# Optimization experiments

Hardware: AMD Instinct MI355X
Metric: run time of the kernel (lower is better)

Reference implementation:

```python
import jax, jax.numpy as jnp
import numpy as np

NUM_LAYERS = 3
DROPOUT = 0.0  # set to 0 for deterministic reference (torch F.dropout uses its own RNG)


def _spmm(rows, cols, vals, X, n_rows):
    # sparse [n_rows, n_cols] @ X[n_cols, D] via gather + segment_sum
    return jax.ops.segment_sum(vals[:, None] * X[cols], rows, num_segments=n_rows)


def setup_inputs() -> dict:
    key = jax.random.key(0)
    k1, k2, k3, k4, k5 = jax.random.split(key, 5)
    P, U, NNZ, D = 100000, 50000, 2000000, 128
    pois_embs = jax.random.normal(k1, (P, D), dtype=jnp.float32)
    up_rows = jax.random.randint(k2, (NNZ,), 0, U, dtype=jnp.int32)
    up_cols = jax.random.randint(k3, (NNZ,), 0, P, dtype=jnp.int32)
    up_vals = jax.random.uniform(k4, (NNZ,), dtype=jnp.float32)
    pu_vals = jax.random.uniform(k5, (NNZ,), dtype=jnp.float32)
    return {
        "pois_embs": pois_embs,
        "pad_all_train_sessions": jnp.zeros((1,), dtype=jnp.int64),
        "up_rows": up_rows,
        "up_cols": up_cols,
        "up_vals": up_vals,
        "pu_vals": pu_vals,
        "n_users": U,
        "n_pois": P,
    }


def reference(pois_embs, pad_all_train_sessions, up_rows, up_cols, up_vals, pu_vals, n_users, n_pois):
    # HG_up: [U, P] with entries (up_rows, up_cols, up_vals)
    # HG_pu: [P, U] = transpose structure with values pu_vals
    x = pois_embs
    acc = pois_embs  # running sum over layer outputs (incl. layer 0)
    for _ in range(NUM_LAYERS):
        msg = _spmm(up_rows, up_cols, up_vals, x, n_users)          # [U, D]
        prop = _spmm(up_cols, up_rows, pu_vals, msg, n_pois)        # [P, D]
        x = prop + x                                                 # residual
        # dropout with p=DROPOUT=0.0 -> identity
        acc = acc + x
    return acc / jnp.asarray(NUM_LAYERS + 1, dtype=pois_embs.dtype)
```

## Files before the change

### kernel.cpp

```cpp
#include <hip/hip_runtime.h>

#define DD 128
#define NUM_LAYERS 3
#define SCAN_B 1024
#define BKT_SHIFT 7
#define BKT_ROWS 128
#define LDS_BKT 1280
#define EPB 4096
#define SHARDS 4
#define CAP_SUB 1792

typedef unsigned int uint;

__device__ __forceinline__ uint f2bf(float f) {
    uint u = __float_as_uint(f);
    return (u + 0x7fffu + ((u >> 16) & 1u)) >> 16;
}
__device__ __forceinline__ uint pk2(float a, float b) {
    return f2bf(a) | (f2bf(b) << 16);
}
__device__ __forceinline__ void fma8(float acc[8], uint4 q, float v) {
    acc[0] += v * __uint_as_float(q.x << 16);
    acc[1] += v * __uint_as_float(q.x & 0xffff0000u);
    acc[2] += v * __uint_as_float(q.y << 16);
    acc[3] += v * __uint_as_float(q.y & 0xffff0000u);
    acc[4] += v * __uint_as_float(q.z << 16);
    acc[5] += v * __uint_as_float(q.z & 0xffff0000u);
    acc[6] += v * __uint_as_float(q.w << 16);
    acc[7] += v * __uint_as_float(q.w & 0xffff0000u);
}


__global__ void pass1_kernel(const int* __restrict__ up_rows,
                             const int* __restrict__ up_cols,
                             const float* __restrict__ up_vals,
                             const float* __restrict__ pu_vals,
                             int* __restrict__ bkcur,
                             int2* __restrict__ stage,
                             int nnz, int U, int nbkt) {
    __shared__ int lcnt[LDS_BKT];
    const int tid = threadIdx.x;
    const int e0 = blockIdx.x * EPB;
    const int shard = blockIdx.x & (SHARDS - 1);
    for (int i = tid; i < nbkt; i += 256) lcnt[i] = 0;
    __syncthreads();
    #pragma unroll
    for (int i = 0; i < EPB / 256; ++i) {
        const int e = e0 + i * 256 + tid;
        if (e < nnz) {
            atomicAdd(&lcnt[up_rows[e] >> BKT_SHIFT], 1);
            atomicAdd(&lcnt[(U + up_cols[e]) >> BKT_SHIFT], 1);
        }
    }
    __syncthreads();
    for (int i = tid; i < nbkt; i += 256) {
        const int c = lcnt[i];
        lcnt[i] = c ? atomicAdd(&bkcur[i * SHARDS + shard], c) : 0;
    }
    __syncthreads();
    #pragma unroll
    for (int i = 0; i < EPB / 256; ++i) {
        const int e = e0 + i * 256 + tid;
        if (e < nnz) {
            const int u = up_rows[e];
            const int p = up_cols[e];
            const int pc = U + p;
            int b = u >> BKT_SHIFT;
            int pos = atomicAdd(&lcnt[b], 1);
            if (pos < CAP_SUB)
                stage[((size_t)b * SHARDS + shard) * CAP_SUB + pos] =
                    make_int2(((u & (BKT_ROWS - 1)) << 25) | p, __float_as_int(up_vals[e]));
            b = pc >> BKT_SHIFT;
            pos = atomicAdd(&lcnt[b], 1);
            if (pos < CAP_SUB)
                stage[((size_t)b * SHARDS + shard) * CAP_SUB + pos] =
                    make_int2(((pc & (BKT_ROWS - 1)) << 25) | u, __float_as_int(pu_vals[e]));
        }
    }
}

__global__ void hist2_kernel(const int* __restrict__ bkcur,
                             const int2* __restrict__ stage,
                             int* __restrict__ cnt, int N) {
    __shared__ int lc[BKT_ROWS];
    const int b = blockIdx.x;
    if (threadIdx.x < BKT_ROWS) lc[threadIdx.x] = 0;
    __syncthreads();
    for (int s = 0; s < SHARDS; ++s) {
        const int n = min(bkcur[b * SHARDS + s], CAP_SUB);
        const int2* bs = stage + ((size_t)b * SHARDS + s) * CAP_SUB;
        for (int i = threadIdx.x; i < n; i += blockDim.x)
            atomicAdd(&lc[((uint)bs[i].x) >> 25], 1);
    }
    __syncthreads();
    const int r = b * BKT_ROWS + threadIdx.x;
    if (threadIdx.x < BKT_ROWS && r < N) cnt[r] = lc[threadIdx.x];
}

__global__ void scan_blocks_kernel(const int* __restrict__ in, int* __restrict__ out,
                                   int* __restrict__ bsums, int n) {
    __shared__ int tmp[SCAN_B];
    const int tid = threadIdx.x;
    const int gid = blockIdx.x * SCAN_B + tid;
    const int v = (gid < n) ? in[gid] : 0;
    tmp[tid] = v;
    __syncthreads();
    for (int ofs = 1; ofs < SCAN_B; ofs <<= 1) {
        int t = (tid >= ofs) ? tmp[tid - ofs] : 0;
        __syncthreads();
        tmp[tid] += t;
        __syncthreads();
    }
    if (gid < n) out[gid] = tmp[tid] - v;
    if (tid == SCAN_B - 1) bsums[blockIdx.x] = tmp[tid];
}

__global__ void scan_sums_kernel(int* __restrict__ bsums, int nb) {
    __shared__ int tmp[SCAN_B];
    const int tid = threadIdx.x;
    const int v = (tid < nb) ? bsums[tid] : 0;
    tmp[tid] = v;
    __syncthreads();
    for (int ofs = 1; ofs < SCAN_B; ofs <<= 1) {
        int t = (tid >= ofs) ? tmp[tid - ofs] : 0;
        __syncthreads();
        tmp[tid] += t;
        __syncthreads();
    }
    if (tid < nb) bsums[tid] = tmp[tid] - v;
}

__global__ void scan_add_kernel(int* __restrict__ off, const int* __restrict__ bsums,
                                const int* __restrict__ cnt, int n) {
    const int gid = blockIdx.x * SCAN_B + threadIdx.x;
    if (gid >= n) return;
    const int v = off[gid] + bsums[blockIdx.x];
    off[gid] = v;
    if (gid == n - 1) off[n] = v + cnt[gid];
}

__global__ void pass2_kernel(const int* __restrict__ bkcur,
                             const int2* __restrict__ stage,
                             const int* __restrict__ off,
                             int2* __restrict__ adj, int N) {
    __shared__ int lcur[BKT_ROWS];
    const int b = blockIdx.x;
    const int r = b * BKT_ROWS + threadIdx.x;
    if (threadIdx.x < BKT_ROWS) lcur[threadIdx.x] = (r < N) ? off[r] : 0;
    __syncthreads();
    for (int s = 0; s < SHARDS; ++s) {
        const int n = min(bkcur[b * SHARDS + s], CAP_SUB);
        const int2* bs = stage + ((size_t)b * SHARDS + s) * CAP_SUB;
        for (int i = threadIdx.x; i < n; i += blockDim.x) {
            const int2 ev = bs[i];
            const uint rl = ((uint)ev.x) >> 25;
            const int col = ev.x & 0x1ffffff;
            const int pos = atomicAdd(&lcur[rl], 1);
            adj[pos] = make_int2(col, ev.y);
        }
    }
}

__global__ void cvt_kernel(const float4* __restrict__ src, uint2* __restrict__ dst, int n4) {
    const int i = blockIdx.x * blockDim.x + threadIdx.x;
    if (i >= n4) return;
    const float4 f = src[i];
    dst[i] = make_uint2(pk2(f.x, f.y), pk2(f.z, f.w));
}


__global__ void spmm_u_kernel(const int* __restrict__ off,
                              const int2* __restrict__ adj,
                              const uint4* __restrict__ xbf,
                              uint4* __restrict__ msgbf, int U) {
    const int g = threadIdx.x >> 4;
    const int lane = threadIdx.x & 15;
    const int row = blockIdx.x * 16 + g;
    if (row >= U) return;
    int k = off[row];
    const int end = off[row + 1];
    float acc[8] = {0, 0, 0, 0, 0, 0, 0, 0};
    for (; k + 1 < end; k += 2) {
        const int2 e0 = adj[k];
        const int2 e1 = adj[k + 1];
        const uint4 q0 = xbf[(size_t)e0.x * 16 + lane];
        const uint4 q1 = xbf[(size_t)e1.x * 16 + lane];
        fma8(acc, q0, __int_as_float(e0.y));
        fma8(acc, q1, __int_as_float(e1.y));
    }
    if (k < end) {
        const int2 e0 = adj[k];
        const uint4 q0 = xbf[(size_t)e0.x * 16 + lane];
        fma8(acc, q0, __int_as_float(e0.y));
    }
    uint4 o;
    o.x = pk2(acc[0], acc[1]);
    o.y = pk2(acc[2], acc[3]);
    o.z = pk2(acc[4], acc[5]);
    o.w = pk2(acc[6], acc[7]);
    msgbf[(size_t)row * 16 + lane] = o;
}

__global__ void spmm_p_fused_kernel(const int* __restrict__ off,
                                    const int2* __restrict__ adj,
                                    const uint4* __restrict__ msgbf,
                                    uint4* __restrict__ xbf,
                                    const float4* __restrict__ embs,
                                    float4* __restrict__ out,
                                    float w, int first, int last, int U, int P) {
    const int g = threadIdx.x >> 4;
    const int lane = threadIdx.x & 15;
    const int row = blockIdx.x * 16 + g;
    if (row >= P) return;
    int k = off[U + row];
    const int end = off[U + row + 1];
    float acc[8] = {0, 0, 0, 0, 0, 0, 0, 0};
    for (; k + 1 < end; k += 2) {
        const int2 e0 = adj[k];
        const int2 e1 = adj[k + 1];
        const uint4 q0 = msgbf[(size_t)e0.x * 16 + lane];
        const uint4 q1 = msgbf[(size_t)e1.x * 16 + lane];
        fma8(acc, q0, __int_as_float(e0.y));
        fma8(acc, q1, __int_as_float(e1.y));
    }
    if (k < end) {
        const int2 e0 = adj[k];
        const uint4 q0 = msgbf[(size_t)e0.x * 16 + lane];
        fma8(acc, q0, __int_as_float(e0.y));
    }
    const size_t xi = (size_t)row * 16 + lane;
    if (!last) {
        const uint4 xq = xbf[xi];
        uint4 xn;
        xn.x = pk2(__uint_as_float(xq.x << 16) + acc[0],
                   __uint_as_float(xq.x & 0xffff0000u) + acc[1]);
        xn.y = pk2(__uint_as_float(xq.y << 16) + acc[2],
                   __uint_as_float(xq.y & 0xffff0000u) + acc[3]);
        xn.z = pk2(__uint_as_float(xq.z << 16) + acc[4],
                   __uint_as_float(xq.z & 0xffff0000u) + acc[5]);
        xn.w = pk2(__uint_as_float(xq.w << 16) + acc[6],
                   __uint_as_float(xq.w & 0xffff0000u) + acc[7]);
        xbf[xi] = xn;
    }
    const size_t oi = (size_t)row * 32 + lane * 2;
    const float4* base = first ? embs : (const float4*)out;
    float4 a = base[oi];
    float4 b = base[oi + 1];
    a.x += w * acc[0]; a.y += w * acc[1]; a.z += w * acc[2]; a.w += w * acc[3];
    b.x += w * acc[4]; b.y += w * acc[5]; b.z += w * acc[6]; b.w += w * acc[7];
    out[oi] = a;
    out[oi + 1] = b;
}


extern "C" void kernel_launch(void* const* d_in, const int* in_sizes, int n_in,
                              void* d_out, int out_size, void* d_ws, size_t ws_size,
                              hipStream_t stream) {
    const float* embs    = (const float*)d_in[0];
    const int*   up_rows = (const int*)d_in[2];
    const int*   up_cols = (const int*)d_in[3];
    const float* up_vals = (const float*)d_in[4];
    const float* pu_vals = (const float*)d_in[5];

    const int NNZ = in_sizes[2];
    const int P   = in_sizes[0] / DD;
    const int U   = 50000;
    const int N   = U + P;
    const int NBKT = (N + BKT_ROWS - 1) / BKT_ROWS;

    float* out = (float*)d_out;

    char* ws = (char*)d_ws;
    size_t o = 0;
    auto alloc = [&](size_t bytes) { size_t r = o; o = (o + bytes + 255) & ~255ULL; return r; };
    int*  bkcur = (int*) (ws + alloc((size_t)NBKT * SHARDS * 4));
    int*  cnt   = (int*) (ws + alloc((size_t)N * 4));
    int*  off   = (int*) (ws + alloc((size_t)(N + 1) * 4));
    int*  bsums = (int*) (ws + alloc((size_t)SCAN_B * 4));
    int2* adj   = (int2*)(ws + alloc((size_t)2 * NNZ * 8));
    const size_t stage_off = alloc((size_t)NBKT * SHARDS * CAP_SUB * 8);
    int2*  stage = (int2*)(ws + stage_off);
    uint4* xbf   = (uint4*)(ws + stage_off);
    uint4* msgbf = (uint4*)(ws + stage_off + (size_t)P * DD * 2);

    const int NB = (N + SCAN_B - 1) / SCAN_B;

    hipMemsetAsync(bkcur, 0, (size_t)NBKT * SHARDS * 4, stream);
    const int p1blocks = (NNZ + EPB - 1) / EPB;
    pass1_kernel<<<p1blocks, 256, 0, stream>>>(up_rows, up_cols, up_vals, pu_vals,
                                               bkcur, stage, NNZ, U, NBKT);
    hist2_kernel<<<NBKT, 256, 0, stream>>>(bkcur, stage, cnt, N);
    scan_blocks_kernel<<<NB, SCAN_B, 0, stream>>>(cnt, off, bsums, N);
    scan_sums_kernel<<<1, SCAN_B, 0, stream>>>(bsums, NB);
    scan_add_kernel<<<NB, SCAN_B, 0, stream>>>(off, bsums, cnt, N);
    pass2_kernel<<<NBKT, 256, 0, stream>>>(bkcur, stage, off, adj, N);

    const int n4 = P * DD / 4;
    cvt_kernel<<<(n4 + 255) / 256, 256, 0, stream>>>((const float4*)embs, (uint2*)xbf, n4);

    const int ublocks = (U + 15) / 16;
    const int pblocks = (P + 15) / 16;

    for (int layer = 0; layer < NUM_LAYERS; ++layer) {
        const float w = (float)(NUM_LAYERS - layer) / (NUM_LAYERS + 1);
        spmm_u_kernel<<<ublocks, 256, 0, stream>>>(off, adj, xbf, msgbf, U);
        spmm_p_fused_kernel<<<pblocks, 256, 0, stream>>>(
            off, adj, msgbf, xbf, (const float4*)embs, (float4*)out,
            w, layer == 0, layer == NUM_LAYERS - 1, U, P);
    }
}
```

Before: 605.6 us.

## Scan per-bucket totals and fuse row histogram into pass2; unroll SpMM gathers by four

Removes the separate per-row histogram pass over the staged edges. The global scan now runs over bucket totals (about 1.2K entries instead of 150K rows), and pass2 computes its per-row counts and local prefix in LDS, writing the CSR offsets itself. The SpMM row loops are also unrolled from 2 to 4 gathers to put more loads in flight, at the cost of more registers per thread. Stage is still read twice, but both reads now happen inside one kernel.

```diff
diff --git a/kernel.cpp b/kernel.cpp
--- a/kernel.cpp
+++ b/kernel.cpp
@@ -79,22 +79,14 @@
     }
 }
 
-__global__ void hist2_kernel(const int* __restrict__ bkcur,
-                             const int2* __restrict__ stage,
-                             int* __restrict__ cnt, int N) {
-    __shared__ int lc[BKT_ROWS];
-    const int b = blockIdx.x;
-    if (threadIdx.x < BKT_ROWS) lc[threadIdx.x] = 0;
-    __syncthreads();
-    for (int s = 0; s < SHARDS; ++s) {
-        const int n = min(bkcur[b * SHARDS + s], CAP_SUB);
-        const int2* bs = stage + ((size_t)b * SHARDS + s) * CAP_SUB;
-        for (int i = threadIdx.x; i < n; i += blockDim.x)
-            atomicAdd(&lc[((uint)bs[i].x) >> 25], 1);
-    }
-    __syncthreads();
-    const int r = b * BKT_ROWS + threadIdx.x;
-    if (threadIdx.x < BKT_ROWS && r < N) cnt[r] = lc[threadIdx.x];
+
+__global__ void tot_kernel(const int* __restrict__ bkcur, int* __restrict__ tot, int nbkt) {
+    const int b = blockIdx.x * blockDim.x + threadIdx.x;
+    if (b >= nbkt) return;
+    int t = 0;
+    #pragma unroll
+    for (int s = 0; s < SHARDS; ++s) t += min(bkcur[b * SHARDS + s], CAP_SUB);
+    tot[b] = t;
 }
 
 __global__ void scan_blocks_kernel(const int* __restrict__ in, int* __restrict__ out,
@@ -139,26 +131,52 @@
     if (gid == n - 1) off[n] = v + cnt[gid];
 }
 
+
 __global__ void pass2_kernel(const int* __restrict__ bkcur,
                              const int2* __restrict__ stage,
-                             const int* __restrict__ off,
-                             int2* __restrict__ adj, int N) {
-    __shared__ int lcur[BKT_ROWS];
+                             const int* __restrict__ bkbase,
+                             int* __restrict__ off,
+                             int2* __restrict__ adj, int N, int nbkt) {
+    __shared__ int ca[BKT_ROWS], cb[BKT_ROWS], lcur[BKT_ROWS];
     const int b = blockIdx.x;
-    const int r = b * BKT_ROWS + threadIdx.x;
-    if (threadIdx.x < BKT_ROWS) lcur[threadIdx.x] = (r < N) ? off[r] : 0;
-    __syncthreads();
+    const int tid = threadIdx.x;
+    if (tid < BKT_ROWS) ca[tid] = 0;
+    __syncthreads();
+    int ns[SHARDS];
+    const int2* bs[SHARDS];
+    #pragma unroll
     for (int s = 0; s < SHARDS; ++s) {
-        const int n = min(bkcur[b * SHARDS + s], CAP_SUB);
-        const int2* bs = stage + ((size_t)b * SHARDS + s) * CAP_SUB;
-        for (int i = threadIdx.x; i < n; i += blockDim.x) {
-            const int2 ev = bs[i];
-            const uint rl = ((uint)ev.x) >> 25;
-            const int col = ev.x & 0x1ffffff;
-            const int pos = atomicAdd(&lcur[rl], 1);
-            adj[pos] = make_int2(col, ev.y);
+        ns[s] = min(bkcur[b * SHARDS + s], CAP_SUB);
+        bs[s] = stage + ((size_t)b * SHARDS + s) * CAP_SUB;
+    }
+    #pragma unroll
+    for (int s = 0; s < SHARDS; ++s)
+        for (int i = tid; i < ns[s]; i += 256)
+            atomicAdd(&ca[((uint)bs[s][i].x) >> 25], 1);
+    __syncthreads();
+    int* src = ca; int* dst = cb;
+    for (int ofs = 1; ofs < BKT_ROWS; ofs <<= 1) {
+        if (tid < BKT_ROWS)
+            dst[tid] = src[tid] + (tid >= ofs ? src[tid - ofs] : 0);
+        __syncthreads();
+        int* t = src; src = dst; dst = t;
+    }
+    const int base = bkbase[b];
+    if (tid < BKT_ROWS) {
+        const int excl = base + (tid ? src[tid - 1] : 0);
+        lcur[tid] = excl;
+        const int r = b * BKT_ROWS + tid;
+        if (r < N) off[r] = excl;
+    }
+    if (b == 0 && tid == 0) off[N] = bkbase[nbkt];
+    __syncthreads();
+    #pragma unroll
+    for (int s = 0; s < SHARDS; ++s)
+        for (int i = tid; i < ns[s]; i += 256) {
+            const int2 ev = bs[s][i];
+            const int pos = atomicAdd(&lcur[((uint)ev.x) >> 25], 1);
+            adj[pos] = make_int2(ev.x & 0x1ffffff, ev.y);
         }
-    }
 }
 
 __global__ void cvt_kernel(const float4* __restrict__ src, uint2* __restrict__ dst, int n4) {
@@ -180,18 +198,24 @@
     int k = off[row];
     const int end = off[row + 1];
     float acc[8] = {0, 0, 0, 0, 0, 0, 0, 0};
-    for (; k + 1 < end; k += 2) {
+    for (; k + 3 < end; k += 4) {
         const int2 e0 = adj[k];
         const int2 e1 = adj[k + 1];
+        const int2 e2 = adj[k + 2];
+        const int2 e3 = adj[k + 3];
         const uint4 q0 = xbf[(size_t)e0.x * 16 + lane];
         const uint4 q1 = xbf[(size_t)e1.x * 16 + lane];
+        const uint4 q2 = xbf[(size_t)e2.x * 16 + lane];
+        const uint4 q3 = xbf[(size_t)e3.x * 16 + lane];
         fma8(acc, q0, __int_as_float(e0.y));
         fma8(acc, q1, __int_as_float(e1.y));
-    }
-    if (k < end) {
-        const int2 e0 = adj[k];
-        const uint4 q0 = xbf[(size_t)e0.x * 16 + lane];
-        fma8(acc, q0, __int_as_float(e0.y));
+        fma8(acc, q2, __int_as_float(e2.y));
+        fma8(acc, q3, __int_as_float(e3.y));
+    }
+    for (; k < end; ++k) {
+        const int2 e = adj[k];
+        const uint4 q = xbf[(size_t)e.x * 16 + lane];
+        fma8(acc, q, __int_as_float(e.y));
     }
     uint4 o;
     o.x = pk2(acc[0], acc[1]);
@@ -215,18 +239,24 @@
     int k = off[U + row];
     const int end = off[U + row + 1];
     float acc[8] = {0, 0, 0, 0, 0, 0, 0, 0};
-    for (; k + 1 < end; k += 2) {
+    for (; k + 3 < end; k += 4) {
         const int2 e0 = adj[k];
         const int2 e1 = adj[k + 1];
+        const int2 e2 = adj[k + 2];
+        const int2 e3 = adj[k + 3];
         const uint4 q0 = msgbf[(size_t)e0.x * 16 + lane];
         const uint4 q1 = msgbf[(size_t)e1.x * 16 + lane];
+        const uint4 q2 = msgbf[(size_t)e2.x * 16 + lane];
+        const uint4 q3 = msgbf[(size_t)e3.x * 16 + lane];
         fma8(acc, q0, __int_as_float(e0.y));
         fma8(acc, q1, __int_as_float(e1.y));
-    }
-    if (k < end) {
-        const int2 e0 = adj[k];
-        const uint4 q0 = msgbf[(size_t)e0.x * 16 + lane];
-        fma8(acc, q0, __int_as_float(e0.y));
+        fma8(acc, q2, __int_as_float(e2.y));
+        fma8(acc, q3, __int_as_float(e3.y));
+    }
+    for (; k < end; ++k) {
+        const int2 e = adj[k];
+        const uint4 q = msgbf[(size_t)e.x * 16 + lane];
+        fma8(acc, q, __int_as_float(e.y));
     }
     const size_t xi = (size_t)row * 16 + lane;
     if (!last) {
@@ -273,27 +303,27 @@
     char* ws = (char*)d_ws;
     size_t o = 0;
     auto alloc = [&](size_t bytes) { size_t r = o; o = (o + bytes + 255) & ~255ULL; return r; };
-    int*  bkcur = (int*) (ws + alloc((size_t)NBKT * SHARDS * 4));
-    int*  cnt   = (int*) (ws + alloc((size_t)N * 4));
-    int*  off   = (int*) (ws + alloc((size_t)(N + 1) * 4));
-    int*  bsums = (int*) (ws + alloc((size_t)SCAN_B * 4));
-    int2* adj   = (int2*)(ws + alloc((size_t)2 * NNZ * 8));
+    int*  bkcur  = (int*) (ws + alloc((size_t)NBKT * SHARDS * 4));
+    int*  tot    = (int*) (ws + alloc((size_t)NBKT * 4));
+    int*  bkbase = (int*) (ws + alloc((size_t)(NBKT + 1) * 4));
+    int*  bsums  = (int*) (ws + alloc((size_t)SCAN_B * 4));
+    int*  off    = (int*) (ws + alloc((size_t)(N + 1) * 4));
+    int2* adj    = (int2*)(ws + alloc((size_t)2 * NNZ * 8));
     const size_t stage_off = alloc((size_t)NBKT * SHARDS * CAP_SUB * 8);
     int2*  stage = (int2*)(ws + stage_off);
     uint4* xbf   = (uint4*)(ws + stage_off);
     uint4* msgbf = (uint4*)(ws + stage_off + (size_t)P * DD * 2);
 
-    const int NB = (N + SCAN_B - 1) / SCAN_B;
-
     hipMemsetAsync(bkcur, 0, (size_t)NBKT * SHARDS * 4, stream);
     const int p1blocks = (NNZ + EPB - 1) / EPB;
     pass1_kernel<<<p1blocks, 256, 0, stream>>>(up_rows, up_cols, up_vals, pu_vals,
                                                bkcur, stage, NNZ, U, NBKT);
-    hist2_kernel<<<NBKT, 256, 0, stream>>>(bkcur, stage, cnt, N);
-    scan_blocks_kernel<<<NB, SCAN_B, 0, stream>>>(cnt, off, bsums, N);
-    scan_sums_kernel<<<1, SCAN_B, 0, stream>>>(bsums, NB);
-    scan_add_kernel<<<NB, SCAN_B, 0, stream>>>(off, bsums, cnt, N);
-    pass2_kernel<<<NBKT, 256, 0, stream>>>(bkcur, stage, off, adj, N);
+    tot_kernel<<<(NBKT + 255) / 256, 256, 0, stream>>>(bkcur, tot, NBKT);
+    const int NBb = (NBKT + SCAN_B - 1) / SCAN_B;
+    scan_blocks_kernel<<<NBb, SCAN_B, 0, stream>>>(tot, bkbase, bsums, NBKT);
+    scan_sums_kernel<<<1, SCAN_B, 0, stream>>>(bsums, NBb);
+    scan_add_kernel<<<NBb, SCAN_B, 0, stream>>>(bkbase, bsums, tot, NBKT);
+    pass2_kernel<<<NBKT, 256, 0, stream>>>(bkcur, stage, bkbase, off, adj, N, NBKT);
 
     const int n4 = P * DD / 4;
     cvt_kernel<<<(n4 + 255) / 256, 256, 0, stream>>>((const float4*)embs, (uint2*)xbf, n4);
```

Result: faster. 579.5 us (-4.3%).
